# Performance work log

Hardware: AMD Instinct MI355X
Metric: run time of the kernel (lower is better)

## Reference

```python
import jax, jax.numpy as jnp
import numpy as np
from jax import lax

IC, OC, K = 512, 512, 3
EPS = 1e-8
BLUR = np.array([1.0, 3.0, 3.0, 1.0], dtype=np.float32)


def setup_inputs() -> dict:
    key = jax.random.key(0)
    k1, k2 = jax.random.split(key)
    x = jax.random.normal(k1, (1, IC, 128, 128), dtype=jnp.float32)
    weight = jax.random.normal(k2, (1, OC, IC, K, K), dtype=jnp.float32)
    return {"x": x, "weight": weight}


def _blur_kernel():
    k1d = BLUR / BLUR.sum()  # normalize before outer product is equiv (sum of outer = 1)
    k2d = np.outer(k1d, k1d)
    k2d = k2d / k2d.sum()
    k2d = k2d * 4.0  # upsample_factor ** 2
    return jnp.asarray(k2d, dtype=jnp.float32)


def reference(x, weight):
    # x: (1, IC, H, W); weight: (1, OC, IC, K, K)
    scale = 1.0 / np.sqrt(IC * K * K)
    w = scale * weight
    # demodulation (batch = 1)
    demod = lax.rsqrt(jnp.sum(w * w, axis=(2, 3, 4)) + EPS)  # (1, OC)
    w = w * demod[:, :, None, None, None]
    w = w[0]  # (OC, IC, K, K)

    # conv_transpose2d(stride=2, padding=0) == conv with lhs_dilation=2,
    # spatial pad K-1, and spatially-flipped kernel.
    wt = jnp.flip(w, axis=(2, 3))  # (OC, IC, K, K)
    out = lax.conv_general_dilated(
        x, wt,
        window_strides=(1, 1),
        padding=[(K - 1, K - 1), (K - 1, K - 1)],
        lhs_dilation=(2, 2),
        dimension_numbers=("NCHW", "OIHW", "NCHW"),
    )  # (1, OC, 2H+1, 2W+1) = (1, 512, 257, 257)

    # Blur: depthwise FIR filter, pad0 = pad1 = 1, kernel 4x4 (upfirdn2d flips kernel)
    bk = jnp.flip(_blur_kernel(), axis=(0, 1))  # (4, 4), symmetric so flip is a no-op
    bkern = jnp.broadcast_to(bk[None, None], (OC, 1, 4, 4))
    out = lax.conv_general_dilated(
        out, bkern,
        window_strides=(1, 1),
        padding=[(1, 1), (1, 1)],
        feature_group_count=OC,
        dimension_numbers=("NCHW", "OIHW", "NCHW"),
    )  # (1, OC, 256, 256)
    return out
```

## Files before the change

### kernel.cpp

```cpp
#include <hip/hip_runtime.h>
#include <hip/hip_bf16.h>

#define ICN 512
#define OCN 512
#define RS    136
#define NROW  17792
#define GUARD 144
#define XROWS 17936

typedef __attribute__((ext_vector_type(8))) short short8;
typedef __attribute__((ext_vector_type(4))) float f32x4;

__device__ __forceinline__ void gload_lds16(const void* g, void* l) {
  __builtin_amdgcn_global_load_lds(
      (const __attribute__((address_space(1))) void*)g,
      (__attribute__((address_space(3))) void*)l, 16, 0, 0);
}

__device__ __forceinline__ void bar_raw() {
  asm volatile("" ::: "memory");
  __builtin_amdgcn_s_barrier();
  asm volatile("" ::: "memory");
}

__global__ __launch_bounds__(256) void wprep_k(const float* __restrict__ w,
                                               __hip_bfloat16* __restrict__ AP) {
  constexpr int WIDX[9] = {0, 2, 6, 8, 1, 7, 3, 5, 4};
  const int oc = blockIdx.x;
  const int tid = threadIdx.x, lane = tid & 63, wv = tid >> 6;

  float v[2][9];
  float s = 0.f;
#pragma unroll
  for (int rep = 0; rep < 2; ++rep) {
    const int ic = tid + rep * 256;
    const float* wp = w + ((size_t)oc * ICN + ic) * 9;
#pragma unroll
    for (int j = 0; j < 9; ++j) { v[rep][j] = wp[j]; s += wp[j] * wp[j]; }
  }
#pragma unroll
  for (int o = 32; o > 0; o >>= 1) s += __shfl_down(s, o, 64);
  __shared__ float red[4];
  if (lane == 0) red[wv] = s;
  __syncthreads();
  const float tot = red[0] + red[1] + red[2] + red[3];
  const float scale2 = 1.0f / 4608.0f;
  const float c = sqrtf(scale2) * rsqrtf(scale2 * tot + 1e-8f);

#pragma unroll
  for (int rep = 0; rep < 2; ++rep) {
    const int ic = tid + rep * 256;
#pragma unroll
    for (int tp = 0; tp < 9; ++tp)
      AP[((size_t)tp * OCN + oc) * ICN + ic] = __float2bfloat16(c * v[rep][WIDX[tp]]);
  }
}

__global__ __launch_bounds__(256) void packx2_k(const float* __restrict__ x,
                                                unsigned int* __restrict__ XP32) {
  const int py  = blockIdx.x;
  const int ic0 = blockIdx.y * 64;
  const int tid = threadIdx.x;
  const int yy  = py - 1;
  const bool rowvalid = (unsigned)yy < 128u;

  __shared__ __hip_bfloat16 T[128 * 65];

  if (rowvalid) {
    const float4* xr = (const float4*)(x + (size_t)ic0 * 16384 + (size_t)yy * 128);
#pragma unroll
    for (int rep = 0; rep < 8; ++rep) {
      const int idx = rep * 256 + tid;
      const int x4 = idx & 31, ici = idx >> 5;
      const float4 v = xr[(size_t)ici * 4096 + x4];
      const int xx = x4 * 4;
      T[(xx + 0) * 65 + ici] = __float2bfloat16(v.x);
      T[(xx + 1) * 65 + ici] = __float2bfloat16(v.y);
      T[(xx + 2) * 65 + ici] = __float2bfloat16(v.z);
      T[(xx + 3) * 65 + ici] = __float2bfloat16(v.w);
    }
  }
  __syncthreads();

  const size_t rowbase = (size_t)(GUARD + py * 136) * 256 + (ic0 >> 1);
  for (int rep = 0; rep < 17; ++rep) {
    const int idx = rep * 256 + tid;
    const int px = idx >> 5, j = idx & 31;
    unsigned int uv = 0;
    if (rowvalid && (unsigned)(px - 1) < 128u) {
      union { __hip_bfloat16 h[2]; unsigned int u; } cv;
      cv.h[0] = T[(px - 1) * 65 + 2 * j];
      cv.h[1] = T[(px - 1) * 65 + 2 * j + 1];
      uv = cv.u;
    }
    XP32[rowbase + (size_t)px * 256 + j] = uv;
  }
}

__global__ __launch_bounds__(256) void zguard_k(unsigned int* __restrict__ XP32) {
  const int r = blockIdx.x;
  const int row = (r < 144) ? r : (r + 17680);
  XP32[(size_t)row * 256 + threadIdx.x] = 0;
}

__global__ __launch_bounds__(512, 2) void gemm_k(const __hip_bfloat16* __restrict__ AP,
                                                 const __hip_bfloat16* __restrict__ XPT,
                                                 __hip_bfloat16* __restrict__ C) {
  constexpr int NTt[4]   = {4, 2, 2, 1};
  constexpr int TPO[4]   = {0, 4, 6, 8};
  constexpr int SHIFT[9] = {0, 1, 136, 137, 0, 136, 0, 1, 0};
  constexpr int AR[4]    = {129, 129, 128, 128};
  constexpr int AC[4]    = {129, 128, 129, 128};

  const int n0 = blockIdx.x * 256, oc0 = blockIdx.y * 256, ph = blockIdx.z;
  const int tid = threadIdx.x, lane = tid & 63, wv = tid >> 6;
  const int wr = wv >> 2, wc = wv & 3;
  const int klane = (lane >> 4) * 16;

  __shared__ __align__(16) char lds[3 * 32768];

  const int T = NTt[ph] * 16;

  auto STAGE = [&](int ts, int buf) {
    const int tp = TPO[ph] + (ts >> 4);
    const size_t kt64 = (size_t)(ts & 15) * 64;
    const char* Ab = (const char*)AP + (size_t)tp * (512 * 1024) +
                     (size_t)oc0 * 1024 + kt64;
    const char* Bb = (const char*)XPT +
                     (size_t)(GUARD + n0 - SHIFT[tp]) * 1024 + kt64;
    char* L = lds + buf * 32768;
#pragma unroll
    for (int o = 0; o < 2; ++o) {
      const int d = o * 8192 + tid * 16;
      const int s = d ^ (((d >> 6) & 3) << 4);
      gload_lds16(Ab + (s >> 6) * 1024 + (s & 63), L + o * 8192 + wv * 1024);
    }
#pragma unroll
    for (int o = 0; o < 2; ++o) {
      const int d = o * 8192 + tid * 16;
      const int s = d ^ (((d >> 6) & 3) << 4);
      gload_lds16(Bb + (s >> 6) * 1024 + (s & 63),
                  L + 16384 + o * 8192 + wv * 1024);
    }
  };

  f32x4 acc[8][4];
#pragma unroll
  for (int m = 0; m < 8; ++m)
#pragma unroll
    for (int n = 0; n < 4; ++n) acc[m][n] = (f32x4){0.f, 0.f, 0.f, 0.f};

  STAGE(0, 0);
  STAGE(1, 1);

  for (int t = 0; t < T; ++t) {
    const int ts = (t + 2 < T) ? (t + 2) : (T - 1);
    STAGE(ts, (t + 2) % 3);
    asm volatile("s_waitcnt vmcnt(8)" ::: "memory");
    __builtin_amdgcn_sched_barrier(0);
    bar_raw();

    const char* LA = lds + (t % 3) * 32768;
    const char* LB = LA + 16384;
    short8 bf[4], af[8];
#pragma unroll
    for (int n = 0; n < 4; ++n) {
      const int b = (wc * 64 + n * 16 + (lane & 15)) * 64 + klane;
      bf[n] = *(const short8*)(LB + (b ^ (((b >> 6) & 3) << 4)));
    }
#pragma unroll
    for (int m = 0; m < 8; ++m) {
      const int a = (wr * 128 + m * 16 + (lane & 15)) * 64 + klane;
      af[m] = *(const short8*)(LA + (a ^ (((a >> 6) & 3) << 4)));
    }
    asm volatile("s_waitcnt lgkmcnt(4)");
    __builtin_amdgcn_sched_barrier(0);
    __builtin_amdgcn_s_setprio(1);
#pragma unroll
    for (int m = 0; m < 4; ++m)
#pragma unroll
      for (int n = 0; n < 4; ++n)
        acc[m][n] = __builtin_amdgcn_mfma_f32_16x16x32_bf16(af[m], bf[n], acc[m][n], 0, 0, 0);
    asm volatile("s_waitcnt lgkmcnt(0)");
    __builtin_amdgcn_sched_barrier(0);
#pragma unroll
    for (int m = 4; m < 8; ++m)
#pragma unroll
      for (int n = 0; n < 4; ++n)
        acc[m][n] = __builtin_amdgcn_mfma_f32_16x16x32_bf16(af[m], bf[n], acc[m][n], 0, 0, 0);
    __builtin_amdgcn_s_setprio(0);
    asm volatile("s_waitcnt lgkmcnt(0)" ::: "memory");
    bar_raw();
  }

  const int lr = (lane >> 4) * 4, lc = lane & 15;
#pragma unroll
  for (int n = 0; n < 4; ++n) {
    const int col = n0 + wc * 64 + n * 16 + lc;
    if (col < NROW) {
      const int pa = col / 136, pb = col - pa * 136;
      const bool ok = ((unsigned)(pa - 1) < (unsigned)AR[ph]) &&
                      ((unsigned)(pb - 1) < (unsigned)AC[ph]);
#pragma unroll
      for (int m = 0; m < 8; ++m)
#pragma unroll
        for (int r = 0; r < 4; ++r) {
          const int row = oc0 + wr * 128 + m * 16 + lr + r;
          C[((size_t)(ph * OCN + row)) * NROW + col] =
              __float2bfloat16(ok ? acc[m][n][r] : 0.f);
        }
    }
  }
}

struct __align__(8) U4 { unsigned int w[4]; };

__global__ __launch_bounds__(256) void blur2_k(const unsigned short* __restrict__ C,
                                               float* __restrict__ out) {
  const int tid = threadIdx.x;
  const int t  = tid & 31;
  const int m  = blockIdx.x * 8 + (tid >> 5);
  const int oc = blockIdx.y;
  const float cfv[4] = {0.25f, 0.75f, 0.75f, 0.25f};

  float acc[8];
#pragma unroll
  for (int s = 0; s < 8; ++s) acc[s] = 0.f;

#pragma unroll
  for (int i = 0; i < 4; ++i) {
    const int u  = m - 1 + i;
    const int py = u & 1;
    const int r  = (u >> 1) + 1;
    const size_t base = (size_t)r * 136 + 4 * t;
    const U4 ev = *(const U4*)(C + ((size_t)(py * 2 + 0) * OCN + oc) * NROW + base);
    const U4 ov = *(const U4*)(C + ((size_t)(py * 2 + 1) * OCN + oc) * NROW + base);
    float E[8], O[8];
#pragma unroll
    for (int j = 0; j < 4; ++j) {
      E[2 * j]     = __uint_as_float(ev.w[j] << 16);
      E[2 * j + 1] = __uint_as_float(ev.w[j] & 0xffff0000u);
      O[2 * j]     = __uint_as_float(ov.w[j] << 16);
      O[2 * j + 1] = __uint_as_float(ov.w[j] & 0xffff0000u);
    }
    const float cv = cfv[i];
#pragma unroll
    for (int s = 0; s < 8; ++s) {
      float h;
      if ((s & 1) == 0) {
        const int k = s >> 1;
        h = 0.75f * E[k + 1] + 0.25f * E[k + 2] + 0.25f * O[k] + 0.75f * O[k + 1];
      } else {
        const int k = (s + 1) >> 1;
        h = 0.25f * E[k] + 0.75f * E[k + 1] + 0.75f * O[k] + 0.25f * O[k + 1];
      }
      acc[s] += cv * h;
    }
  }

  float* op = out + ((size_t)oc * 256 + m) * 256 + 8 * t;
  f32x4 s0 = {acc[0], acc[1], acc[2], acc[3]};
  f32x4 s1 = {acc[4], acc[5], acc[6], acc[7]};
  *(f32x4*)op = s0;
  *(f32x4*)(op + 4) = s1;
}

extern "C" void kernel_launch(void* const* d_in, const int* in_sizes, int n_in,
                              void* d_out, int out_size, void* d_ws, size_t ws_size,
                              hipStream_t stream) {
  const float* x = (const float*)d_in[0];
  const float* w = (const float*)d_in[1];
  float* out = (float*)d_out;

  __hip_bfloat16* AP  = (__hip_bfloat16*)d_ws;
  __hip_bfloat16* XPT = (__hip_bfloat16*)((char*)d_ws + 4718592);
  __hip_bfloat16* C   = (__hip_bfloat16*)((char*)d_ws + 23085056);

  wprep_k<<<512, 256, 0, stream>>>(w, AP);
  zguard_k<<<256, 256, 0, stream>>>((unsigned int*)XPT);
  packx2_k<<<dim3(130, 8), 256, 0, stream>>>(x, (unsigned int*)XPT);
  gemm_k<<<dim3(70, 2, 4), 512, 0, stream>>>(AP, XPT, C);
  blur2_k<<<dim3(32, 512), 256, 0, stream>>>((const unsigned short*)C, out);
}
```

Measured before the change: 165.0 us.

## Restructure GEMM mainloop to K=128 double-buffered tiles with ping-pong MFMA phases

```diff
diff --git a/kernel.cpp b/kernel.cpp
--- a/kernel.cpp
+++ b/kernel.cpp
@@ -115,33 +115,32 @@
   const int n0 = blockIdx.x * 256, oc0 = blockIdx.y * 256, ph = blockIdx.z;
   const int tid = threadIdx.x, lane = tid & 63, wv = tid >> 6;
   const int wr = wv >> 2, wc = wv & 3;
-  const int klane = (lane >> 4) * 16;
-
-  __shared__ __align__(16) char lds[3 * 32768];
-
-  const int T = NTt[ph] * 16;
-
-  auto STAGE = [&](int ts, int buf) {
-    const int tp = TPO[ph] + (ts >> 4);
-    const size_t kt64 = (size_t)(ts & 15) * 64;
-    const char* Ab = (const char*)AP + (size_t)tp * (512 * 1024) +
-                     (size_t)oc0 * 1024 + kt64;
-    const char* Bb = (const char*)XPT +
-                     (size_t)(GUARD + n0 - SHIFT[tp]) * 1024 + kt64;
-    char* L = lds + buf * 32768;
-#pragma unroll
-    for (int o = 0; o < 2; ++o) {
-      const int d = o * 8192 + tid * 16;
-      const int s = d ^ (((d >> 6) & 3) << 4);
-      gload_lds16(Ab + (s >> 6) * 1024 + (s & 63), L + o * 8192 + wv * 1024);
-    }
-#pragma unroll
-    for (int o = 0; o < 2; ++o) {
-      const int d = o * 8192 + tid * 16;
-      const int s = d ^ (((d >> 6) & 3) << 4);
-      gload_lds16(Bb + (s >> 6) * 1024 + (s & 63),
-                  L + 16384 + o * 8192 + wv * 1024);
-    }
+  const int lane15 = lane & 15, l7 = lane & 7;
+  const int kx = (lane >> 4) * 16;
+
+  __shared__ __align__(16) char lds[2 * 65536];
+
+  const int T = NTt[ph] * 8;
+
+  auto STAGE = [&](int i, char* Lb) {
+    const int tp = TPO[ph] + (i >> 3);
+    const size_t kb = (size_t)(i & 7) * 128;
+    const char* Ag = (const char*)AP + (size_t)tp * (512 * 1024) +
+                     (size_t)oc0 * 1024 + kb;
+    const char* Bg = (const char*)XPT +
+                     (size_t)(GUARD + n0 - SHIFT[tp]) * 1024 + kb;
+#pragma unroll
+    for (int hh = 0; hh < 2; ++hh)
+#pragma unroll
+      for (int c = 0; c < 2; ++c) {
+        const int d = c * 8192 + tid * 16;
+        const int r = d >> 7;
+        const int wk = (d & 127) ^ ((r & 7) << 4);
+        gload_lds16(Ag + (size_t)(hh * 128 + r) * 1024 + wk,
+                    Lb + hh * 16384 + c * 8192 + wv * 1024);
+        gload_lds16(Bg + (size_t)(hh * 128 + r) * 1024 + wk,
+                    Lb + 32768 + hh * 16384 + c * 8192 + wv * 1024);
+      }
   };
 
   f32x4 acc[8][4];
@@ -150,46 +149,110 @@
 #pragma unroll
     for (int n = 0; n < 4; ++n) acc[m][n] = (f32x4){0.f, 0.f, 0.f, 0.f};
 
-  STAGE(0, 0);
-  STAGE(1, 1);
+  STAGE(0, lds);
+  asm volatile("s_waitcnt vmcnt(0)" ::: "memory");
+  bar_raw();
 
   for (int t = 0; t < T; ++t) {
-    const int ts = (t + 2 < T) ? (t + 2) : (T - 1);
-    STAGE(ts, (t + 2) % 3);
-    asm volatile("s_waitcnt vmcnt(8)" ::: "memory");
-    __builtin_amdgcn_sched_barrier(0);
-    bar_raw();
-
-    const char* LA = lds + (t % 3) * 32768;
-    const char* LB = LA + 16384;
-    short8 bf[4], af[8];
-#pragma unroll
-    for (int n = 0; n < 4; ++n) {
-      const int b = (wc * 64 + n * 16 + (lane & 15)) * 64 + klane;
-      bf[n] = *(const short8*)(LB + (b ^ (((b >> 6) & 3) << 4)));
-    }
-#pragma unroll
-    for (int m = 0; m < 8; ++m) {
-      const int a = (wr * 128 + m * 16 + (lane & 15)) * 64 + klane;
-      af[m] = *(const short8*)(LA + (a ^ (((a >> 6) & 3) << 4)));
-    }
-    asm volatile("s_waitcnt lgkmcnt(4)");
+    const int buf = t & 1;
+    const char* LA = lds + buf * 65536 + wr * 16384;
+    const char* LB = lds + buf * 65536 + 32768 + (wc >> 1) * 16384;
+    const int brow = (wc & 1) * 64;
+
+    short8 bf[4][2], afA[2][2], afB[2][2];
+
+#pragma unroll
+    for (int n = 0; n < 4; ++n)
+#pragma unroll
+      for (int kh = 0; kh < 2; ++kh) {
+        const int e = (brow + n * 16 + lane15) * 128 + kh * 64 + kx;
+        bf[n][kh] = *(const short8*)(LB + (e ^ (l7 << 4)));
+      }
+#pragma unroll
+    for (int j = 0; j < 2; ++j)
+#pragma unroll
+      for (int kh = 0; kh < 2; ++kh) {
+        const int e = ((0 + j) * 16 + lane15) * 128 + kh * 64 + kx;
+        afA[j][kh] = *(const short8*)(LA + (e ^ (l7 << 4)));
+      }
+    if (t + 1 < T) STAGE(t + 1, lds + (buf ^ 1) * 65536);
+    bar_raw();
+    asm volatile("s_waitcnt lgkmcnt(0)");
     __builtin_amdgcn_sched_barrier(0);
     __builtin_amdgcn_s_setprio(1);
 #pragma unroll
-    for (int m = 0; m < 4; ++m)
-#pragma unroll
-      for (int n = 0; n < 4; ++n)
-        acc[m][n] = __builtin_amdgcn_mfma_f32_16x16x32_bf16(af[m], bf[n], acc[m][n], 0, 0, 0);
+    for (int j = 0; j < 2; ++j)
+#pragma unroll
+      for (int kh = 0; kh < 2; ++kh)
+#pragma unroll
+        for (int n = 0; n < 4; ++n)
+          acc[0 + j][n] = __builtin_amdgcn_mfma_f32_16x16x32_bf16(afA[j][kh], bf[n][kh], acc[0 + j][n], 0, 0, 0);
+    __builtin_amdgcn_s_setprio(0);
+    bar_raw();
+
+#pragma unroll
+    for (int j = 0; j < 2; ++j)
+#pragma unroll
+      for (int kh = 0; kh < 2; ++kh) {
+        const int e = ((2 + j) * 16 + lane15) * 128 + kh * 64 + kx;
+        afB[j][kh] = *(const short8*)(LA + (e ^ (l7 << 4)));
+      }
+    bar_raw();
     asm volatile("s_waitcnt lgkmcnt(0)");
     __builtin_amdgcn_sched_barrier(0);
-#pragma unroll
-    for (int m = 4; m < 8; ++m)
-#pragma unroll
-      for (int n = 0; n < 4; ++n)
-        acc[m][n] = __builtin_amdgcn_mfma_f32_16x16x32_bf16(af[m], bf[n], acc[m][n], 0, 0, 0);
+    __builtin_amdgcn_s_setprio(1);
+#pragma unroll
+    for (int j = 0; j < 2; ++j)
+#pragma unroll
+      for (int kh = 0; kh < 2; ++kh)
+#pragma unroll
+        for (int n = 0; n < 4; ++n)
+          acc[2 + j][n] = __builtin_amdgcn_mfma_f32_16x16x32_bf16(afB[j][kh], bf[n][kh], acc[2 + j][n], 0, 0, 0);
     __builtin_amdgcn_s_setprio(0);
-    asm volatile("s_waitcnt lgkmcnt(0)" ::: "memory");
+    bar_raw();
+
+#pragma unroll
+    for (int j = 0; j < 2; ++j)
+#pragma unroll
+      for (int kh = 0; kh < 2; ++kh) {
+        const int e = ((4 + j) * 16 + lane15) * 128 + kh * 64 + kx;
+        afA[j][kh] = *(const short8*)(LA + (e ^ (l7 << 4)));
+      }
+    bar_raw();
+    asm volatile("s_waitcnt lgkmcnt(0)");
+    __builtin_amdgcn_sched_barrier(0);
+    __builtin_amdgcn_s_setprio(1);
+#pragma unroll
+    for (int j = 0; j < 2; ++j)
+#pragma unroll
+      for (int kh = 0; kh < 2; ++kh)
+#pragma unroll
+        for (int n = 0; n < 4; ++n)
+          acc[4 + j][n] = __builtin_amdgcn_mfma_f32_16x16x32_bf16(afA[j][kh], bf[n][kh], acc[4 + j][n], 0, 0, 0);
+    __builtin_amdgcn_s_setprio(0);
+    bar_raw();
+
+#pragma unroll
+    for (int j = 0; j < 2; ++j)
+#pragma unroll
+      for (int kh = 0; kh < 2; ++kh) {
+        const int e = ((6 + j) * 16 + lane15) * 128 + kh * 64 + kx;
+        afB[j][kh] = *(const short8*)(LA + (e ^ (l7 << 4)));
+      }
+    bar_raw();
+    asm volatile("s_waitcnt lgkmcnt(0)");
+    __builtin_amdgcn_sched_barrier(0);
+    __builtin_amdgcn_s_setprio(1);
+#pragma unroll
+    for (int j = 0; j < 2; ++j)
+#pragma unroll
+      for (int kh = 0; kh < 2; ++kh)
+#pragma unroll
+        for (int n = 0; n < 4; ++n)
+          acc[6 + j][n] = __builtin_amdgcn_mfma_f32_16x16x32_bf16(afB[j][kh], bf[n][kh], acc[6 + j][n], 0, 0, 0);
+    __builtin_amdgcn_s_setprio(0);
+    asm volatile("s_waitcnt vmcnt(0)" ::: "memory");
+    __builtin_amdgcn_sched_barrier(0);
     bar_raw();
   }
 
```

Measured after the change: 155.1 us. 1.06x faster.

## Restructure GEMM main loop: double-buffered 128-wide K tiles with interleaved loads

Applied to the files above, without the earlier changes.

```diff
diff --git a/kernel.cpp b/kernel.cpp
--- a/kernel.cpp
+++ b/kernel.cpp
@@ -22,6 +22,8 @@
   __builtin_amdgcn_s_barrier();
   asm volatile("" ::: "memory");
 }
+
+#define SB0() __builtin_amdgcn_sched_barrier(0)
 
 __global__ __launch_bounds__(256) void wprep_k(const float* __restrict__ w,
                                                __hip_bfloat16* __restrict__ AP) {
@@ -115,33 +117,24 @@
   const int n0 = blockIdx.x * 256, oc0 = blockIdx.y * 256, ph = blockIdx.z;
   const int tid = threadIdx.x, lane = tid & 63, wv = tid >> 6;
   const int wr = wv >> 2, wc = wv & 3;
-  const int klane = (lane >> 4) * 16;
-
-  __shared__ __align__(16) char lds[3 * 32768];
-
-  const int T = NTt[ph] * 16;
-
-  auto STAGE = [&](int ts, int buf) {
-    const int tp = TPO[ph] + (ts >> 4);
-    const size_t kt64 = (size_t)(ts & 15) * 64;
-    const char* Ab = (const char*)AP + (size_t)tp * (512 * 1024) +
-                     (size_t)oc0 * 1024 + kt64;
-    const char* Bb = (const char*)XPT +
-                     (size_t)(GUARD + n0 - SHIFT[tp]) * 1024 + kt64;
-    char* L = lds + buf * 32768;
-#pragma unroll
-    for (int o = 0; o < 2; ++o) {
-      const int d = o * 8192 + tid * 16;
-      const int s = d ^ (((d >> 6) & 3) << 4);
-      gload_lds16(Ab + (s >> 6) * 1024 + (s & 63), L + o * 8192 + wv * 1024);
-    }
-#pragma unroll
-    for (int o = 0; o < 2; ++o) {
-      const int d = o * 8192 + tid * 16;
-      const int s = d ^ (((d >> 6) & 3) << 4);
-      gload_lds16(Bb + (s >> 6) * 1024 + (s & 63),
-                  L + 16384 + o * 8192 + wv * 1024);
-    }
+  const int lane15 = lane & 15, l7 = lane & 7;
+  const int kx = (lane >> 4) * 16;
+
+  __shared__ __align__(16) char lds[2 * 65536];
+
+  const int T = NTt[ph] * 8;
+
+  const int r0  = tid >> 3;
+  const int wk0 = ((tid * 16) & 127) ^ ((r0 & 7) << 4);
+
+  auto STG = [&](const char* Ag, const char* Bg, char* Lnext, int g) {
+    const int hh = (g >> 1) & 1, c = g & 1;
+    if (g < 4)
+      gload_lds16(Ag + (size_t)(hh * 128 + r0 + c * 64) * 1024 + wk0,
+                  Lnext + hh * 16384 + c * 8192 + wv * 1024);
+    else
+      gload_lds16(Bg + (size_t)(hh * 128 + r0 + c * 64) * 1024 + wk0,
+                  Lnext + 32768 + hh * 16384 + c * 8192 + wv * 1024);
   };
 
   f32x4 acc[8][4];
@@ -150,48 +143,115 @@
 #pragma unroll
     for (int n = 0; n < 4; ++n) acc[m][n] = (f32x4){0.f, 0.f, 0.f, 0.f};
 
-  STAGE(0, 0);
-  STAGE(1, 1);
+  {
+    const int tp = TPO[ph];
+    const char* Ag = (const char*)AP + (size_t)tp * (512 * 1024) + (size_t)oc0 * 1024;
+    const char* Bg = (const char*)XPT + (size_t)(GUARD + n0 - SHIFT[tp]) * 1024;
+#pragma unroll
+    for (int g = 0; g < 8; ++g) STG(Ag, Bg, lds, g);
+  }
+  asm volatile("s_waitcnt vmcnt(0)" ::: "memory");
+  bar_raw();
+
+#define DSR(dst, base, row, khh)                                            \
+  { const int e_ = (row) * 128 + (khh) * 64 + kx;                           \
+    dst = *(const short8*)((base) + (e_ ^ (l7 << 4))); }
+
+#define MFMA8(mb, afv, bfv)                                                 \
+  _Pragma("unroll") for (int j = 0; j < 2; ++j)                             \
+  _Pragma("unroll") for (int n = 0; n < 4; ++n)                             \
+    acc[(mb) + j][n] = __builtin_amdgcn_mfma_f32_16x16x32_bf16(             \
+        afv[j], bfv[n], acc[(mb) + j][n], 0, 0, 0);
 
   for (int t = 0; t < T; ++t) {
-    const int ts = (t + 2 < T) ? (t + 2) : (T - 1);
-    STAGE(ts, (t + 2) % 3);
-    asm volatile("s_waitcnt vmcnt(8)" ::: "memory");
-    __builtin_amdgcn_sched_barrier(0);
+    const int buf = t & 1;
+    const char* LA = lds + buf * 65536 + wr * 16384;
+    const char* LB = lds + buf * 65536 + 32768 + (wc >> 1) * 16384;
+    const int brow = (wc & 1) * 64;
+    char* Lnext = lds + (buf ^ 1) * 65536;
+    const int ts = (t + 1 < T) ? (t + 1) : (T - 1);
+    const int tp = TPO[ph] + (ts >> 3);
+    const size_t kb = (size_t)(ts & 7) * 128;
+    const char* Ag = (const char*)AP + (size_t)tp * (512 * 1024) +
+                     (size_t)oc0 * 1024 + kb;
+    const char* Bg = (const char*)XPT +
+                     (size_t)(GUARD + n0 - SHIFT[tp]) * 1024 + kb;
+
+    short8 bf0[4], bf1[4], afA[2], afB[2];
+
+#pragma unroll
+    for (int n = 0; n < 4; ++n) DSR(bf0[n], LB, brow + n * 16 + lane15, 0);
+    DSR(afA[0], LA, 0 * 16 + lane15, 0);
+    DSR(afA[1], LA, 1 * 16 + lane15, 0);
+    SB0();
+#pragma unroll
+    for (int n = 0; n < 4; ++n) DSR(bf1[n], LB, brow + n * 16 + lane15, 1);
+    DSR(afB[0], LA, 0 * 16 + lane15, 1);
+    DSR(afB[1], LA, 1 * 16 + lane15, 1);
+    SB0();
+    asm volatile("s_waitcnt lgkmcnt(6)");
+    SB0();
+    __builtin_amdgcn_s_setprio(1); MFMA8(0, afA, bf0); __builtin_amdgcn_s_setprio(0);
+    SB0(); STG(Ag, Bg, Lnext, 0); STG(Ag, Bg, Lnext, 1); SB0();
+
+    DSR(afA[0], LA, 2 * 16 + lane15, 0);
+    DSR(afA[1], LA, 3 * 16 + lane15, 0);
+    SB0();
+    asm volatile("s_waitcnt lgkmcnt(2)");
+    SB0();
+    __builtin_amdgcn_s_setprio(1); MFMA8(0, afB, bf1); __builtin_amdgcn_s_setprio(0);
+    SB0(); STG(Ag, Bg, Lnext, 2); STG(Ag, Bg, Lnext, 3); SB0();
+
+    DSR(afB[0], LA, 2 * 16 + lane15, 1);
+    DSR(afB[1], LA, 3 * 16 + lane15, 1);
+    SB0();
+    asm volatile("s_waitcnt lgkmcnt(2)");
+    SB0();
+    __builtin_amdgcn_s_setprio(1); MFMA8(2, afA, bf0); __builtin_amdgcn_s_setprio(0);
+    SB0(); STG(Ag, Bg, Lnext, 4); STG(Ag, Bg, Lnext, 5); SB0();
+
+    DSR(afA[0], LA, 4 * 16 + lane15, 0);
+    DSR(afA[1], LA, 5 * 16 + lane15, 0);
+    SB0();
+    asm volatile("s_waitcnt lgkmcnt(2)");
+    SB0();
+    __builtin_amdgcn_s_setprio(1); MFMA8(2, afB, bf1); __builtin_amdgcn_s_setprio(0);
+    SB0(); STG(Ag, Bg, Lnext, 6); STG(Ag, Bg, Lnext, 7); SB0();
+
+    DSR(afB[0], LA, 4 * 16 + lane15, 1);
+    DSR(afB[1], LA, 5 * 16 + lane15, 1);
+    SB0();
+    asm volatile("s_waitcnt lgkmcnt(2)");
+    SB0();
+    __builtin_amdgcn_s_setprio(1); MFMA8(4, afA, bf0); __builtin_amdgcn_s_setprio(0);
+    SB0();
+
+    DSR(afA[0], LA, 6 * 16 + lane15, 0);
+    DSR(afA[1], LA, 7 * 16 + lane15, 0);
+    SB0();
+    asm volatile("s_waitcnt lgkmcnt(2)");
+    SB0();
+    __builtin_amdgcn_s_setprio(1); MFMA8(4, afB, bf1); __builtin_amdgcn_s_setprio(0);
+    SB0();
+
+    DSR(afB[0], LA, 6 * 16 + lane15, 1);
+    DSR(afB[1], LA, 7 * 16 + lane15, 1);
+    SB0();
+    asm volatile("s_waitcnt lgkmcnt(2)");
+    SB0();
+    __builtin_amdgcn_s_setprio(1); MFMA8(6, afA, bf0); __builtin_amdgcn_s_setprio(0);
+    SB0();
+
+    asm volatile("s_waitcnt lgkmcnt(0)");
+    SB0();
+    __builtin_amdgcn_s_setprio(1); MFMA8(6, afB, bf1); __builtin_amdgcn_s_setprio(0);
+
+    asm volatile("s_waitcnt vmcnt(0)" ::: "memory");
+    SB0();
     bar_raw();
-
-    const char* LA = lds + (t % 3) * 32768;
-    const char* LB = LA + 16384;
-    short8 bf[4], af[8];
-#pragma unroll
-    for (int n = 0; n < 4; ++n) {
-      const int b = (wc * 64 + n * 16 + (lane & 15)) * 64 + klane;
-      bf[n] = *(const short8*)(LB + (b ^ (((b >> 6) & 3) << 4)));
-    }
-#pragma unroll
-    for (int m = 0; m < 8; ++m) {
-      const int a = (wr * 128 + m * 16 + (lane & 15)) * 64 + klane;
-      af[m] = *(const short8*)(LA + (a ^ (((a >> 6) & 3) << 4)));
-    }
-    asm volatile("s_waitcnt lgkmcnt(4)");
-    __builtin_amdgcn_sched_barrier(0);
-    __builtin_amdgcn_s_setprio(1);
-#pragma unroll
-    for (int m = 0; m < 4; ++m)
-#pragma unroll
-      for (int n = 0; n < 4; ++n)
-        acc[m][n] = __builtin_amdgcn_mfma_f32_16x16x32_bf16(af[m], bf[n], acc[m][n], 0, 0, 0);
-    asm volatile("s_waitcnt lgkmcnt(0)");
-    __builtin_amdgcn_sched_barrier(0);
-#pragma unroll
-    for (int m = 4; m < 8; ++m)
-#pragma unroll
-      for (int n = 0; n < 4; ++n)
-        acc[m][n] = __builtin_amdgcn_mfma_f32_16x16x32_bf16(af[m], bf[n], acc[m][n], 0, 0, 0);
-    __builtin_amdgcn_s_setprio(0);
-    asm volatile("s_waitcnt lgkmcnt(0)" ::: "memory");
-    bar_raw();
-  }
+  }
+#undef DSR
+#undef MFMA8
 
   const int lr = (lane >> 4) * 4, lc = lane & 15;
 #pragma unroll
```

New measurement: 146.2 us (median of 2 runs). -11.4%, faster.

## Software-pipeline LDS fragment reads with MFMA and drop a per-iteration barrier

Applied to the files above, without the earlier changes.

```diff
diff --git a/kernel.cpp b/kernel.cpp
--- a/kernel.cpp
+++ b/kernel.cpp
@@ -22,6 +22,8 @@
   __builtin_amdgcn_s_barrier();
   asm volatile("" ::: "memory");
 }
+
+#define SB0() __builtin_amdgcn_sched_barrier(0)
 
 __global__ __launch_bounds__(256) void wprep_k(const float* __restrict__ w,
                                                __hip_bfloat16* __restrict__ AP) {
@@ -115,32 +117,29 @@
   const int n0 = blockIdx.x * 256, oc0 = blockIdx.y * 256, ph = blockIdx.z;
   const int tid = threadIdx.x, lane = tid & 63, wv = tid >> 6;
   const int wr = wv >> 2, wc = wv & 3;
-  const int klane = (lane >> 4) * 16;
+  const int lane15 = lane & 15;
+  const int kx = (lane >> 4) * 16;
 
   __shared__ __align__(16) char lds[3 * 32768];
 
-  const int T = NTt[ph] * 16;
-
-  auto STAGE = [&](int ts, int buf) {
-    const int tp = TPO[ph] + (ts >> 4);
-    const size_t kt64 = (size_t)(ts & 15) * 64;
-    const char* Ab = (const char*)AP + (size_t)tp * (512 * 1024) +
-                     (size_t)oc0 * 1024 + kt64;
-    const char* Bb = (const char*)XPT +
-                     (size_t)(GUARD + n0 - SHIFT[tp]) * 1024 + kt64;
-    char* L = lds + buf * 32768;
-#pragma unroll
-    for (int o = 0; o < 2; ++o) {
-      const int d = o * 8192 + tid * 16;
-      const int s = d ^ (((d >> 6) & 3) << 4);
-      gload_lds16(Ab + (s >> 6) * 1024 + (s & 63), L + o * 8192 + wv * 1024);
-    }
-#pragma unroll
-    for (int o = 0; o < 2; ++o) {
-      const int d = o * 8192 + tid * 16;
-      const int s = d ^ (((d >> 6) & 3) << 4);
-      gload_lds16(Bb + (s >> 6) * 1024 + (s & 63),
-                  L + 16384 + o * 8192 + wv * 1024);
+  const int T2 = NTt[ph] * 16;
+
+  const int sr = tid >> 2;
+  const int sc = ((tid & 3) * 16) ^ (((sr >> 1) & 3) << 4);
+
+  auto STG = [&](int i, char* Lb) {
+    const int tp = TPO[ph] + (i >> 4);
+    const size_t kb = (size_t)(i & 15) * 64;
+    const char* Ag = (const char*)AP + (size_t)tp * (512 * 1024) +
+                     (size_t)oc0 * 1024 + kb;
+    const char* Bg = (const char*)XPT +
+                     (size_t)(GUARD + n0 - SHIFT[tp]) * 1024 + kb;
+#pragma unroll
+    for (int g = 0; g < 2; ++g) {
+      gload_lds16(Ag + (size_t)(g * 128 + sr) * 1024 + sc,
+                  Lb + g * 8192 + wv * 1024);
+      gload_lds16(Bg + (size_t)(g * 128 + sr) * 1024 + sc,
+                  Lb + 16384 + g * 8192 + wv * 1024);
     }
   };
 
@@ -150,48 +149,70 @@
 #pragma unroll
     for (int n = 0; n < 4; ++n) acc[m][n] = (f32x4){0.f, 0.f, 0.f, 0.f};
 
-  STAGE(0, 0);
-  STAGE(1, 1);
-
-  for (int t = 0; t < T; ++t) {
-    const int ts = (t + 2 < T) ? (t + 2) : (T - 1);
-    STAGE(ts, (t + 2) % 3);
-    asm volatile("s_waitcnt vmcnt(8)" ::: "memory");
-    __builtin_amdgcn_sched_barrier(0);
+  STG(0, lds);
+  STG(1, lds + 32768);
+  asm volatile("s_waitcnt vmcnt(4)" ::: "memory");
+  bar_raw();
+
+#define DSR(dst, base, row)                                                  \
+  { const int e_ = (row) * 64 + kx;                                          \
+    dst = *(const short8*)((base) + (e_ ^ ((((row) >> 1) & 3) << 4))); }
+
+#define MFMA8(mb, afv)                                                       \
+  _Pragma("unroll") for (int j = 0; j < 2; ++j)                              \
+  _Pragma("unroll") for (int n = 0; n < 4; ++n)                              \
+    acc[(mb) + j][n] = __builtin_amdgcn_mfma_f32_16x16x32_bf16(              \
+        afv[j], bf[n], acc[(mb) + j][n], 0, 0, 0);
+
+  for (int t = 0; t < T2; ++t) {
+    const char* LA = lds + (t % 3) * 32768 + wr * 8192;
+    const char* LB = lds + (t % 3) * 32768 + 16384;
+    char* Ln = lds + ((t + 2) % 3) * 32768;
+    const int ts = (t + 2 < T2) ? (t + 2) : (T2 - 1);
+
+    short8 bf[4], afA[2], afB[2];
+
+#pragma unroll
+    for (int n = 0; n < 4; ++n) DSR(bf[n], LB, wc * 64 + n * 16 + lane15);
+    DSR(afA[0], LA, 0 * 16 + lane15);
+    DSR(afA[1], LA, 1 * 16 + lane15);
+    SB0();
+    STG(ts, Ln);
+    SB0();
+    DSR(afB[0], LA, 2 * 16 + lane15);
+    DSR(afB[1], LA, 3 * 16 + lane15);
+    SB0();
+    asm volatile("s_waitcnt lgkmcnt(2)");
+    SB0();
+    __builtin_amdgcn_s_setprio(1); MFMA8(0, afA); __builtin_amdgcn_s_setprio(0);
+    SB0();
+
+    DSR(afA[0], LA, 4 * 16 + lane15);
+    DSR(afA[1], LA, 5 * 16 + lane15);
+    SB0();
+    asm volatile("s_waitcnt lgkmcnt(2)");
+    SB0();
+    __builtin_amdgcn_s_setprio(1); MFMA8(2, afB); __builtin_amdgcn_s_setprio(0);
+    SB0();
+
+    DSR(afB[0], LA, 6 * 16 + lane15);
+    DSR(afB[1], LA, 7 * 16 + lane15);
+    SB0();
+    asm volatile("s_waitcnt lgkmcnt(2)");
+    SB0();
+    __builtin_amdgcn_s_setprio(1); MFMA8(4, afA); __builtin_amdgcn_s_setprio(0);
+    SB0();
+
+    asm volatile("s_waitcnt lgkmcnt(0)");
+    SB0();
+    __builtin_amdgcn_s_setprio(1); MFMA8(6, afB); __builtin_amdgcn_s_setprio(0);
+
+    asm volatile("s_waitcnt vmcnt(4)" ::: "memory");
+    SB0();
     bar_raw();
-
-    const char* LA = lds + (t % 3) * 32768;
-    const char* LB = LA + 16384;
-    short8 bf[4], af[8];
-#pragma unroll
-    for (int n = 0; n < 4; ++n) {
-      const int b = (wc * 64 + n * 16 + (lane & 15)) * 64 + klane;
-      bf[n] = *(const short8*)(LB + (b ^ (((b >> 6) & 3) << 4)));
-    }
-#pragma unroll
-    for (int m = 0; m < 8; ++m) {
-      const int a = (wr * 128 + m * 16 + (lane & 15)) * 64 + klane;
-      af[m] = *(const short8*)(LA + (a ^ (((a >> 6) & 3) << 4)));
-    }
-    asm volatile("s_waitcnt lgkmcnt(4)");
-    __builtin_amdgcn_sched_barrier(0);
-    __builtin_amdgcn_s_setprio(1);
-#pragma unroll
-    for (int m = 0; m < 4; ++m)
-#pragma unroll
-      for (int n = 0; n < 4; ++n)
-        acc[m][n] = __builtin_amdgcn_mfma_f32_16x16x32_bf16(af[m], bf[n], acc[m][n], 0, 0, 0);
-    asm volatile("s_waitcnt lgkmcnt(0)");
-    __builtin_amdgcn_sched_barrier(0);
-#pragma unroll
-    for (int m = 4; m < 8; ++m)
-#pragma unroll
-      for (int n = 0; n < 4; ++n)
-        acc[m][n] = __builtin_amdgcn_mfma_f32_16x16x32_bf16(af[m], bf[n], acc[m][n], 0, 0, 0);
-    __builtin_amdgcn_s_setprio(0);
-    asm volatile("s_waitcnt lgkmcnt(0)" ::: "memory");
-    bar_raw();
-  }
+  }
+#undef DSR
+#undef MFMA8
 
   const int lr = (lane >> 4) * 4, lc = lane & 15;
 #pragma unroll
```

Result: faster. 153.7 us (-6.9%).
